# Kernel optimization log

Measured on AMD Instinct MI355X. Metric: run time of the kernel, lower is better.

Reference implementation:

```python
import jax, jax.numpy as jnp
import numpy as np

N = 524288      # number of spacetime samples (rays*samples)
E = 16          # num_experts
K = 2           # num_selected_experts
HID = 16        # SpacetimeGeometricMLP hidden_dim (layers are hidden_dim*2 wide)
OUT = 4         # rgb + density


def setup_inputs() -> dict:
    key = jax.random.key(0)
    ks = jax.random.split(key, 8)
    return {
        "xyzt": jax.random.normal(ks[0], (N, 4), jnp.float32),
        # gate: Linear(4, E)
        "Wg": jax.random.normal(ks[1], (4, E), jnp.float32) * 0.5,
        "bg": jnp.zeros((E,), jnp.float32),
        # per-expert SphericalEmbedding params
        "proj": jax.random.normal(ks[2], (E, 3, 8), jnp.float32),
        "center": jax.random.normal(ks[3], (E, 3), jnp.float32) * 0.01,
        # per-expert TimeEmbedding biases
        "tb1": jnp.zeros((E,), jnp.float32),
        "tb2": jnp.zeros((E,), jnp.float32),
        # per-expert feature_mlp Linear(12, 2*HID, bias=False) and final Linear(2*HID, OUT)
        "W1": jax.random.normal(ks[4], (E, 12, 2 * HID), jnp.float32) * (12 ** -0.5),
        "Wf": jax.random.normal(ks[5], (E, 2 * HID, OUT), jnp.float32) * ((2 * HID) ** -0.5),
        "bf": jnp.zeros((E, OUT), jnp.float32),
    }


def _moe_forward(xyzt, Wg, bg, proj, center, tb1, tb2, W1, Wf, bf):
    n = xyzt.shape[0]
    # --- gate: top-k + softmax over selected logits (softmax in fp32, as in torch) ---
    logits = xyzt @ Wg + bg                                   # [N, E]
    w, sel = jax.lax.top_k(logits, K)                         # [N, K]
    w = jax.nn.softmax(w.astype(jnp.float32), axis=1).astype(xyzt.dtype)
    # dense combine weights: zero for unselected experts -> identical math to
    # the torch gather/scatter loop with sum pooling.
    w_dense = jnp.zeros((n, E), xyzt.dtype).at[jnp.arange(n)[:, None], sel].set(w)  # [N, E]

    xyz, t = xyzt[:, :3], xyzt[:, 3:4]

    def expert(proj_e, center_e, tb1_e, tb2_e, W1_e, Wf_e, bf_e):
        # SphericalEmbedding
        xc = xyz - center_e                                   # [N, 3]
        rho = jnp.sqrt(jnp.sum(xc * xc, -1, keepdims=True))   # [N, 1]
        phi = jnp.arctan2(xc[:, 1], xc[:, 0])[:, None]
        theta = jnp.arccos(xc[:, 2] / (rho[:, 0] + 1e-6))[:, None]
        sph = jnp.concatenate([rho, phi, theta], -1) @ proj_e  # [N, 8]
        # TimeEmbedding
        cos_t = jnp.cos(t + tb1_e)
        sin_t = jnp.sin(t + tb2_e)
        temb = jnp.concatenate([cos_t, sin_t, jax.nn.silu(cos_t), jax.nn.silu(sin_t)], -1)  # [N, 4]
        emb = jnp.concatenate([sph, temb], -1)                # [N, 12]
        # feature_mlp (depth=0, no bias) + final_layer
        h = emb @ W1_e                                        # [N, 2*HID]
        return h @ Wf_e + bf_e                                # [N, OUT]

    outs = jax.vmap(expert)(proj, center, tb1, tb2, W1, Wf, bf)  # [E, N, OUT]
    return jnp.einsum('ne,end->nd', w_dense, outs)               # [N, OUT]


def reference(xyzt, Wg, bg, proj, center, tb1, tb2, W1, Wf, bf):
    return _moe_forward(xyzt, Wg, bg, proj, center, tb1, tb2, W1, Wf, bf)
```

## Files before the change

kernel.cpp:

```cpp
#include <hip/hip_runtime.h>
#include <math.h>

#define NE 16
#define WPE 44


__global__ __launch_bounds__(256) void moe_prep_kernel(
        const float* __restrict__ proj,
        const float* __restrict__ center,
        const float* __restrict__ tb1,
        const float* __restrict__ tb2,
        const float* __restrict__ W1,
        const float* __restrict__ Wf,
        const float* __restrict__ bf,
        float* __restrict__ tbl) {
    __shared__ float Msh[NE * 48];
    int t = threadIdx.x;
    {
        int e = t >> 4, l = t & 15;
        #pragma unroll
        for (int k = 0; k < 3; ++k) {
            int j = l + k * 16;
            int i = j >> 2, d = j & 3;
            const float* w1r = W1 + (e * 12 + i) * 32;
            const float* wfc = Wf + e * 128 + d;
            float s = 0.f;
            #pragma unroll
            for (int q = 0; q < 32; ++q) s = fmaf(w1r[q], wfc[q * 4], s);
            Msh[e * 48 + j] = s;
        }
    }
    __syncthreads();
    if (t < NE * 4) {
        int e = t >> 2, d = t & 3;
        const float* Me = Msh + e * 48;
        float* o = tbl + e * WPE;
        #pragma unroll
        for (int j = 0; j < 3; ++j) {
            float s = 0.f;
            const float* pr = proj + e * 24 + j * 8;
            #pragma unroll
            for (int i = 0; i < 8; ++i) s = fmaf(pr[i], Me[i * 4 + d], s);
            o[j * 4 + d] = s;
        }
        #pragma unroll
        for (int i = 0; i < 4; ++i) o[(3 + i) * 4 + d] = Me[(8 + i) * 4 + d];
        o[7 * 4 + d] = bf[e * 4 + d];
        if (d == 0) {
            o[32] = center[e * 3 + 0];
            o[33] = center[e * 3 + 1];
            o[34] = center[e * 3 + 2];
            o[35] = cosf(tb1[e]);
            o[36] = sinf(tb1[e]);
            o[37] = cosf(tb2[e]);
            o[38] = sinf(tb2[e]);
            o[39] = 0.f; o[40] = 0.f; o[41] = 0.f; o[42] = 0.f; o[43] = 0.f;
        }
    }
}

__device__ __forceinline__ float fast_rcp(float x) {
    return __builtin_amdgcn_rcpf(x);
}

__device__ __forceinline__ float4 f4fma(float s, float4 a, float4 b) {
    return make_float4(fmaf(s, a.x, b.x), fmaf(s, a.y, b.y),
                       fmaf(s, a.z, b.z), fmaf(s, a.w, b.w));
}

__device__ __forceinline__ float fast_atan2f(float y, float x) {
    float ax = fabsf(x), ay = fabsf(y);
    float mx = fmaxf(ax, ay), mn = fminf(ax, ay);
    float r = mn * fast_rcp(fmaxf(mx, 1e-37f));
    float s = r * r;
    float p =              -0.0117212f;
    p = fmaf(p, s,  0.05265332f);
    p = fmaf(p, s, -0.11643287f);
    p = fmaf(p, s,  0.19354346f);
    p = fmaf(p, s, -0.33262347f);
    p = fmaf(p, s,  0.99997726f);
    float a = r * p;
    a = (ay > ax) ? (1.57079637f - a) : a;
    a = (x < 0.f) ? (3.14159274f - a) : a;
    return copysignf(a, y);
}

__device__ __forceinline__ float fast_acosf(float x) {
    float ax = fminf(fabsf(x), 1.f);
    float p = fmaf(ax, -0.0187293f, 0.0742610f);
    p = fmaf(p, ax, -0.2121144f);
    p = fmaf(p, ax, 1.5707288f);
    float r = sqrtf(1.f - ax) * p;
    return (x >= 0.f) ? r : (3.14159274f - r);
}

__global__ __launch_bounds__(256) void moe_main_kernel(
        const float4* __restrict__ xyzt,
        const float* __restrict__ Wg,
        const float* __restrict__ bg,
        const float* __restrict__ tbl,
        float4* __restrict__ out, int n) {
    __shared__ float lds[NE * WPE];
    for (int i = threadIdx.x; i < NE * WPE; i += 256) lds[i] = tbl[i];
    __syncthreads();

    int idx = blockIdx.x * 256 + threadIdx.x;
    if (idx >= n) return;
    float4 p = xyzt[idx];

    float logits[NE];
    #pragma unroll
    for (int e = 0; e < NE; ++e) {
        logits[e] = fmaf(p.x, Wg[e],
                    fmaf(p.y, Wg[NE + e],
                    fmaf(p.z, Wg[2 * NE + e],
                    fmaf(p.w, Wg[3 * NE + e], bg[e]))));
    }
    float best = logits[0]; int bi = 0;
    float second = -INFINITY; int si = 0;
    #pragma unroll
    for (int e = 1; e < NE; ++e) {
        float l = logits[e];
        if (l > best)        { second = best; si = bi; best = l; bi = e; }
        else if (l > second) { second = l; si = e; }
    }
    float ed = __expf(second - best);
    float w0 = fast_rcp(1.f + ed);
    float w1 = ed * w0;

    float st, ct;
    __sincosf(p.w, &st, &ct);

    int   sel[2] = { bi, si };
    float wgt[2] = { w0, w1 };
    float4 acc = make_float4(0.f, 0.f, 0.f, 0.f);

    #pragma unroll
    for (int kk = 0; kk < 2; ++kk) {
        const float4* w4 = (const float4*)(lds + sel[kk] * WPE);
        float4 cc = w4[8];
        float4 ss = w4[9];
        float xc0 = p.x - cc.x, xc1 = p.y - cc.y, xc2 = p.z - cc.z;
        float rho = sqrtf(fmaf(xc0, xc0, fmaf(xc1, xc1, xc2 * xc2)));
        float phi = fast_atan2f(xc1, xc0);
        float theta = fast_acosf(xc2 * fast_rcp(rho + 1e-6f));
        float cos_t = fmaf(ct, cc.w, -st * ss.x);
        float sin_t = fmaf(st, ss.y,  ct * ss.z);
        float silc = cos_t * fast_rcp(1.f + __expf(-cos_t));
        float sils = sin_t * fast_rcp(1.f + __expf(-sin_t));

        float4 r = w4[7];
        r = f4fma(rho,   w4[0], r);
        r = f4fma(phi,   w4[1], r);
        r = f4fma(theta, w4[2], r);
        r = f4fma(cos_t, w4[3], r);
        r = f4fma(sin_t, w4[4], r);
        r = f4fma(silc,  w4[5], r);
        r = f4fma(sils,  w4[6], r);
        acc = f4fma(wgt[kk], r, acc);
    }
    out[idx] = acc;
}

extern "C" void kernel_launch(void* const* d_in, const int* in_sizes, int n_in,
                              void* d_out, int out_size, void* d_ws, size_t ws_size,
                              hipStream_t stream) {
    const float* xyzt   = (const float*)d_in[0];
    const float* Wg     = (const float*)d_in[1];
    const float* bg     = (const float*)d_in[2];
    const float* proj   = (const float*)d_in[3];
    const float* center = (const float*)d_in[4];
    const float* tb1    = (const float*)d_in[5];
    const float* tb2    = (const float*)d_in[6];
    const float* W1     = (const float*)d_in[7];
    const float* Wf     = (const float*)d_in[8];
    const float* bf     = (const float*)d_in[9];
    float* tbl = (float*)d_ws;
    int n = in_sizes[0] / 4;

    moe_prep_kernel<<<1, 256, 0, stream>>>(proj, center, tb1, tb2, W1, Wf, bf, tbl);
    moe_main_kernel<<<(n + 255) / 256, 256, 0, stream>>>(
        (const float4*)xyzt, Wg, bg, tbl, (float4*)d_out, n);
}
```

Before: 86.29 us.

## Fuse weight-folding prep into main kernel and process two points per thread

Removes the separate single-block prep kernel and has every block recompute the folded per-expert table (W1·Wf, proj folding, time-bias sin/cos) directly into shared memory. Each thread now handles two samples strided by the grid size, halving the block count. This saves one kernel launch and the serialized dependency between the two kernels, but every block now redundantly does the 32-term dot products and global reads of W1/Wf before starting its real work.

```diff
diff --git a/kernel.cpp b/kernel.cpp
--- a/kernel.cpp
+++ b/kernel.cpp
@@ -3,61 +3,8 @@
 
 #define NE 16
 #define WPE 44
+#define PPT 2
 
-
-__global__ __launch_bounds__(256) void moe_prep_kernel(
-        const float* __restrict__ proj,
-        const float* __restrict__ center,
-        const float* __restrict__ tb1,
-        const float* __restrict__ tb2,
-        const float* __restrict__ W1,
-        const float* __restrict__ Wf,
-        const float* __restrict__ bf,
-        float* __restrict__ tbl) {
-    __shared__ float Msh[NE * 48];
-    int t = threadIdx.x;
-    {
-        int e = t >> 4, l = t & 15;
-        #pragma unroll
-        for (int k = 0; k < 3; ++k) {
-            int j = l + k * 16;
-            int i = j >> 2, d = j & 3;
-            const float* w1r = W1 + (e * 12 + i) * 32;
-            const float* wfc = Wf + e * 128 + d;
-            float s = 0.f;
-            #pragma unroll
-            for (int q = 0; q < 32; ++q) s = fmaf(w1r[q], wfc[q * 4], s);
-            Msh[e * 48 + j] = s;
-        }
-    }
-    __syncthreads();
-    if (t < NE * 4) {
-        int e = t >> 2, d = t & 3;
-        const float* Me = Msh + e * 48;
-        float* o = tbl + e * WPE;
-        #pragma unroll
-        for (int j = 0; j < 3; ++j) {
-            float s = 0.f;
-            const float* pr = proj + e * 24 + j * 8;
-            #pragma unroll
-            for (int i = 0; i < 8; ++i) s = fmaf(pr[i], Me[i * 4 + d], s);
-            o[j * 4 + d] = s;
-        }
-        #pragma unroll
-        for (int i = 0; i < 4; ++i) o[(3 + i) * 4 + d] = Me[(8 + i) * 4 + d];
-        o[7 * 4 + d] = bf[e * 4 + d];
-        if (d == 0) {
-            o[32] = center[e * 3 + 0];
-            o[33] = center[e * 3 + 1];
-            o[34] = center[e * 3 + 2];
-            o[35] = cosf(tb1[e]);
-            o[36] = sinf(tb1[e]);
-            o[37] = cosf(tb2[e]);
-            o[38] = sinf(tb2[e]);
-            o[39] = 0.f; o[40] = 0.f; o[41] = 0.f; o[42] = 0.f; o[43] = 0.f;
-        }
-    }
-}
 
 __device__ __forceinline__ float fast_rcp(float x) {
     return __builtin_amdgcn_rcpf(x);
@@ -94,72 +41,124 @@
     return (x >= 0.f) ? r : (3.14159274f - r);
 }
 
-__global__ __launch_bounds__(256) void moe_main_kernel(
+__global__ __launch_bounds__(256) void moe_fused_kernel(
         const float4* __restrict__ xyzt,
         const float* __restrict__ Wg,
         const float* __restrict__ bg,
-        const float* __restrict__ tbl,
+        const float* __restrict__ proj,
+        const float* __restrict__ center,
+        const float* __restrict__ tb1,
+        const float* __restrict__ tb2,
+        const float* __restrict__ W1,
+        const float* __restrict__ Wf,
+        const float* __restrict__ bf,
         float4* __restrict__ out, int n) {
+    __shared__ float Msh[NE * 48];
     __shared__ float lds[NE * WPE];
-    for (int i = threadIdx.x; i < NE * WPE; i += 256) lds[i] = tbl[i];
+    const int t = threadIdx.x;
+
+    {
+        int e = t >> 4, l = t & 15;
+        #pragma unroll
+        for (int k = 0; k < 3; ++k) {
+            int j = l + k * 16;
+            const float* w1r = W1 + (e * 12 + (j >> 2)) * 32;
+            const float* wfc = Wf + e * 128 + (j & 3);
+            float s = 0.f;
+            #pragma unroll
+            for (int q = 0; q < 32; ++q) s = fmaf(w1r[q], wfc[q * 4], s);
+            Msh[e * 48 + j] = s;
+        }
+    }
+    __syncthreads();
+    if (t < NE * 4) {
+        int e = t >> 2, d = t & 3;
+        const float* Me = Msh + e * 48;
+        float* o = lds + e * WPE;
+        #pragma unroll
+        for (int j = 0; j < 3; ++j) {
+            float s = 0.f;
+            const float* pr = proj + e * 24 + j * 8;
+            #pragma unroll
+            for (int i = 0; i < 8; ++i) s = fmaf(pr[i], Me[i * 4 + d], s);
+            o[j * 4 + d] = s;
+        }
+        #pragma unroll
+        for (int i = 0; i < 4; ++i) o[(3 + i) * 4 + d] = Me[(8 + i) * 4 + d];
+        o[7 * 4 + d] = bf[e * 4 + d];
+        if (d == 0) {
+            o[32] = center[e * 3 + 0];
+            o[33] = center[e * 3 + 1];
+            o[34] = center[e * 3 + 2];
+            o[35] = cosf(tb1[e]);
+            o[36] = sinf(tb1[e]);
+            o[37] = cosf(tb2[e]);
+            o[38] = sinf(tb2[e]);
+            o[39] = 0.f;
+        }
+    }
     __syncthreads();
 
-    int idx = blockIdx.x * 256 + threadIdx.x;
-    if (idx >= n) return;
-    float4 p = xyzt[idx];
+    const int stride = gridDim.x * 256;
+    #pragma unroll
+    for (int pp = 0; pp < PPT; ++pp) {
+        int idx = blockIdx.x * 256 + t + pp * stride;
+        if (idx >= n) continue;
+        float4 p = xyzt[idx];
 
-    float logits[NE];
-    #pragma unroll
-    for (int e = 0; e < NE; ++e) {
-        logits[e] = fmaf(p.x, Wg[e],
-                    fmaf(p.y, Wg[NE + e],
-                    fmaf(p.z, Wg[2 * NE + e],
-                    fmaf(p.w, Wg[3 * NE + e], bg[e]))));
+        float logits[NE];
+        #pragma unroll
+        for (int e = 0; e < NE; ++e) {
+            logits[e] = fmaf(p.x, Wg[e],
+                        fmaf(p.y, Wg[NE + e],
+                        fmaf(p.z, Wg[2 * NE + e],
+                        fmaf(p.w, Wg[3 * NE + e], bg[e]))));
+        }
+        float best = logits[0]; int bi = 0;
+        float second = -INFINITY; int si = 0;
+        #pragma unroll
+        for (int e = 1; e < NE; ++e) {
+            float l = logits[e];
+            if (l > best)        { second = best; si = bi; best = l; bi = e; }
+            else if (l > second) { second = l; si = e; }
+        }
+        float ed = __expf(second - best);
+        float w0 = fast_rcp(1.f + ed);
+        float w1 = ed * w0;
+
+        float st, ct;
+        __sincosf(p.w, &st, &ct);
+
+        int   sel[2] = { bi, si };
+        float wgt[2] = { w0, w1 };
+        float4 acc = make_float4(0.f, 0.f, 0.f, 0.f);
+
+        #pragma unroll
+        for (int kk = 0; kk < 2; ++kk) {
+            const float4* w4 = (const float4*)(lds + sel[kk] * WPE);
+            float4 cc = w4[8];
+            float4 ss = w4[9];
+            float xc0 = p.x - cc.x, xc1 = p.y - cc.y, xc2 = p.z - cc.z;
+            float rho = sqrtf(fmaf(xc0, xc0, fmaf(xc1, xc1, xc2 * xc2)));
+            float phi = fast_atan2f(xc1, xc0);
+            float theta = fast_acosf(xc2 * fast_rcp(rho + 1e-6f));
+            float cos_t = fmaf(ct, cc.w, -st * ss.x);
+            float sin_t = fmaf(st, ss.y,  ct * ss.z);
+            float silc = cos_t * fast_rcp(1.f + __expf(-cos_t));
+            float sils = sin_t * fast_rcp(1.f + __expf(-sin_t));
+
+            float4 r = w4[7];
+            r = f4fma(rho,   w4[0], r);
+            r = f4fma(phi,   w4[1], r);
+            r = f4fma(theta, w4[2], r);
+            r = f4fma(cos_t, w4[3], r);
+            r = f4fma(sin_t, w4[4], r);
+            r = f4fma(silc,  w4[5], r);
+            r = f4fma(sils,  w4[6], r);
+            acc = f4fma(wgt[kk], r, acc);
+        }
+        out[idx] = acc;
     }
-    float best = logits[0]; int bi = 0;
-    float second = -INFINITY; int si = 0;
-    #pragma unroll
-    for (int e = 1; e < NE; ++e) {
-        float l = logits[e];
-        if (l > best)        { second = best; si = bi; best = l; bi = e; }
-        else if (l > second) { second = l; si = e; }
-    }
-    float ed = __expf(second - best);
-    float w0 = fast_rcp(1.f + ed);
-    float w1 = ed * w0;
-
-    float st, ct;
-    __sincosf(p.w, &st, &ct);
-
-    int   sel[2] = { bi, si };
-    float wgt[2] = { w0, w1 };
-    float4 acc = make_float4(0.f, 0.f, 0.f, 0.f);
-
-    #pragma unroll
-    for (int kk = 0; kk < 2; ++kk) {
-        const float4* w4 = (const float4*)(lds + sel[kk] * WPE);
-        float4 cc = w4[8];
-        float4 ss = w4[9];
-        float xc0 = p.x - cc.x, xc1 = p.y - cc.y, xc2 = p.z - cc.z;
-        float rho = sqrtf(fmaf(xc0, xc0, fmaf(xc1, xc1, xc2 * xc2)));
-        float phi = fast_atan2f(xc1, xc0);
-        float theta = fast_acosf(xc2 * fast_rcp(rho + 1e-6f));
-        float cos_t = fmaf(ct, cc.w, -st * ss.x);
-        float sin_t = fmaf(st, ss.y,  ct * ss.z);
-        float silc = cos_t * fast_rcp(1.f + __expf(-cos_t));
-        float sils = sin_t * fast_rcp(1.f + __expf(-sin_t));
-
-        float4 r = w4[7];
-        r = f4fma(rho,   w4[0], r);
-        r = f4fma(phi,   w4[1], r);
-        r = f4fma(theta, w4[2], r);
-        r = f4fma(cos_t, w4[3], r);
-        r = f4fma(sin_t, w4[4], r);
-        r = f4fma(silc,  w4[5], r);
-        r = f4fma(sils,  w4[6], r);
-        acc = f4fma(wgt[kk], r, acc);
-    }
-    out[idx] = acc;
 }
 
 extern "C" void kernel_launch(void* const* d_in, const int* in_sizes, int n_in,
@@ -175,10 +174,11 @@
     const float* W1     = (const float*)d_in[7];
     const float* Wf     = (const float*)d_in[8];
     const float* bf     = (const float*)d_in[9];
-    float* tbl = (float*)d_ws;
     int n = in_sizes[0] / 4;
 
-    moe_prep_kernel<<<1, 256, 0, stream>>>(proj, center, tb1, tb2, W1, Wf, bf, tbl);
-    moe_main_kernel<<<(n + 255) / 256, 256, 0, stream>>>(
-        (const float4*)xyzt, Wg, bg, tbl, (float4*)d_out, n);
+    int threads_needed = (n + PPT - 1) / PPT;
+    int grid = (threads_needed + 255) / 256;
+    moe_fused_kernel<<<grid, 256, 0, stream>>>(
+        (const float4*)xyzt, Wg, bg, proj, center, tb1, tb2, W1, Wf, bf,
+        (float4*)d_out, n);
 }
```

Measured after the change: 90.79 us. +5.2%, slower.
